# Kernel optimization log

Hardware: AMD Instinct MI355X
Metric: run time of the kernel (lower is better)

## Reference

```python
import jax, jax.numpy as jnp
import numpy as np

K = 3  # deformable kernel size
OFFSET_CLIP = 10.0


def _conv2d_same(x, w, b):
    # 3x3 conv, stride 1, padding 1, NCHW/OIHW
    out = jax.lax.conv_general_dilated(
        x, w, window_strides=(1, 1), padding=((1, 1), (1, 1)),
        dimension_numbers=("NCHW", "OIHW", "NCHW"))
    return out + b[None, :, None, None]


def _deform_conv2d(x, offset, weight):
    """torchvision-style deform_conv2d, stride 1, pad 1, dilation 1, no bias.
    x:      [B, C, H, W]
    offset: [B, 2*K*K, H, W]  (per tap: dy then dx)
    weight: [Cout, C, K, K]
    """
    B, C, H, W = x.shape
    off = offset.reshape(B, K * K, 2, H, W)
    ky, kx = jnp.meshgrid(jnp.arange(K, dtype=x.dtype), jnp.arange(K, dtype=x.dtype), indexing="ij")
    ky = ky.reshape(-1)  # [9]
    kx = kx.reshape(-1)
    # sample coords: p0 - pad + k + offset  -> [B, 9, H, W]
    ys = jnp.arange(H, dtype=x.dtype)[None, None, :, None] - 1.0 + ky[None, :, None, None] + off[:, :, 0]
    xs = jnp.arange(W, dtype=x.dtype)[None, None, None, :] - 1.0 + kx[None, :, None, None] + off[:, :, 1]
    y0 = jnp.floor(ys)
    x0 = jnp.floor(xs)
    ty = ys - y0  # fractional parts, [B,9,H,W]
    tx = xs - x0
    iy0 = y0.astype(jnp.int32)
    ix0 = x0.astype(jnp.int32)

    xf = x.reshape(B, C, H * W)

    def gather(iy, ix):
        valid = ((iy >= 0) & (iy < H) & (ix >= 0) & (ix < W)).astype(x.dtype)
        idx = (jnp.clip(iy, 0, H - 1) * W + jnp.clip(ix, 0, W - 1)).reshape(B, -1)
        v = jax.vmap(lambda xv, iv: xv[:, iv])(xf, idx)  # [B, C, 9*H*W]
        return v.reshape(B, C, K * K, H, W) * valid[:, None]

    v00 = gather(iy0, ix0)
    v01 = gather(iy0, ix0 + 1)
    v10 = gather(iy0 + 1, ix0)
    v11 = gather(iy0 + 1, ix0 + 1)

    w00 = ((1.0 - ty) * (1.0 - tx))[:, None]  # [B,1,9,H,W]
    w01 = ((1.0 - ty) * tx)[:, None]
    w10 = (ty * (1.0 - tx))[:, None]
    w11 = (ty * tx)[:, None]

    sampled = v00 * w00 + v01 * w01 + v10 * w10 + v11 * w11  # [B,C,9,H,W]
    return jnp.einsum("bckhw,ock->bohw", sampled, weight.reshape(weight.shape[0], C, K * K))


def setup_inputs() -> dict:
    key = jax.random.key(0)
    k1, k2, k3, k4 = jax.random.split(key, 4)
    B, C, H, W = 4, 64, 128, 128
    x = jax.random.normal(k1, (B, C, H, W), dtype=jnp.float32)
    ref = jax.random.normal(k2, (B, C, H, W), dtype=jnp.float32)
    # offset_conv: in=2C, out=2*3*3=18. (Original zero-inits; we use small random
    # weights so the deformable sampling path is nontrivially exercised.)
    offset_w = jax.random.normal(k3, (2 * K * K, 2 * C, K, K), dtype=jnp.float32) * 0.01
    offset_b = jnp.zeros((2 * K * K,), dtype=jnp.float32)
    # main deform weight: kaiming_normal fan_out, relu -> std = sqrt(2 / (Cout*K*K))
    std = float(np.sqrt(2.0 / (C * K * K)))
    weight = jax.random.normal(k4, (C, C, K, K), dtype=jnp.float32) * std
    return {"x": x, "ref": ref, "offset_w": offset_w, "offset_b": offset_b, "weight": weight}


def reference(x, ref, offset_w, offset_b, weight):
    combined = jnp.concatenate([x, ref], axis=1)
    offset = _conv2d_same(combined, offset_w, offset_b)
    offset = jnp.clip(offset, -OFFSET_CLIP, OFFSET_CLIP)
    aligned = _deform_conv2d(x, offset, weight)
    return aligned.astype(x.dtype)
```

## Files before the change

kernel.cpp:

```cpp
#include <hip/hip_runtime.h>

#define Bsz 4
#define Cch 64
#define Hh 128
#define Ww 128
#define NOFF 18
#define CK 576
#define CKPAD 580

typedef __attribute__((ext_vector_type(8))) short short8;
typedef __attribute__((ext_vector_type(4))) float floatx4;

__device__ __forceinline__ unsigned short f2bf(float f) {
    union { float f; unsigned u; } v; v.f = f;
    unsigned r = v.u + 0x7fff + ((v.u >> 16) & 1);
    return (unsigned short)(r >> 16);
}
__device__ __forceinline__ float bflo(unsigned d) {
    union { unsigned u; float f; } v; v.u = d << 16; return v.f;
}
__device__ __forceinline__ float bfhi(unsigned d) {
    union { unsigned u; float f; } v; v.u = d & 0xffff0000u; return v.f;
}
__device__ __forceinline__ unsigned cvtpk(float lo, float hi) {
    unsigned r;
    asm("v_cvt_pk_bf16_f32 %0, %1, %2" : "=v"(r) : "v"(lo), "v"(hi));
    return r;
}

__global__ __launch_bounds__(256) void prep(const float* __restrict__ x,
                                            const float* __restrict__ ref,
                                            const float* __restrict__ wo,
                                            const float* __restrict__ w,
                                            unsigned* __restrict__ xpair,
                                            unsigned short* __restrict__ w9,
                                            unsigned short* __restrict__ wbf) {
    __shared__ unsigned tile[64][130];
    int bid = blockIdx.x;
    int tid = threadIdx.x;
    if (bid < 512) {
        int b = bid >> 7;
        int h = bid & 127;
        int px2 = tid & 63;
        int cg = tid >> 6;
        const float* xb = x + ((size_t)b << 20) + (h << 7) + (px2 << 1);
        const float* rb = ref + ((size_t)b << 20) + (h << 7) + (px2 << 1);
#pragma unroll
        for (int j = 0; j < 16; ++j) {
            int c0 = cg * 32 + 2 * j;
            const float* s = (c0 < 64) ? xb : rb;
            int cl = c0 & 63;
            float2 va = *(const float2*)(s + ((size_t)cl << 14));
            float2 vb = *(const float2*)(s + ((size_t)(cl + 1) << 14));
            unsigned w0 = (unsigned)f2bf(va.x) | ((unsigned)f2bf(vb.x) << 16);
            unsigned w1 = (unsigned)f2bf(va.y) | ((unsigned)f2bf(vb.y) << 16);
            *(uint2*)(&tile[c0 >> 1][px2 << 1]) = make_uint2(w0, w1);
        }
        __syncthreads();
#pragma unroll
        for (int it = 0; it < 16; ++it) {
            int idx = it * 256 + tid;
            int cq5 = idx & 31;
            int pos = idx >> 5;
            int posn = min(pos + 1, 127);
            unsigned t0 = tile[2 * cq5][pos], t0n = tile[2 * cq5][posn];
            unsigned t1 = tile[2 * cq5 + 1][pos], t1n = tile[2 * cq5 + 1][posn];
            uint4 o;
            o.x = (t0 & 0xffffu) | (t0n << 16);
            o.y = (t0 >> 16) | (t0n & 0xffff0000u);
            o.z = (t1 & 0xffffu) | (t1n << 16);
            o.w = (t1 >> 16) | (t1n & 0xffff0000u);
            *(uint4*)(xpair + (((size_t)(b << 14) + (h << 7) + pos) << 7) + (cq5 << 2)) = o;
        }
    } else if (bid < 656) {
        int t = (bid - 512) * 256 + tid;
        if (t < Cch * CK) {
            int oc = t / CK;
            int rem = t % CK;
            int k = rem >> 6, c = rem & 63;
            wbf[t] = f2bf(w[(oc * Cch + c) * 9 + k]);
        }
    } else {
        int t = (bid - 656) * 256 + tid;
        if (t < 9 * 32 * 128) {
            int ci = t & 127, ocp = (t >> 7) & 31, tap = t >> 12;
            w9[t] = (ocp < NOFF) ? f2bf(wo[(ocp * 128 + ci) * 9 + tap]) : (unsigned short)0;
        }
    }
}

__global__ __launch_bounds__(256, 3) void fused_align(
        const unsigned* __restrict__ xpair,
        const unsigned short* __restrict__ w9,
        const unsigned short* __restrict__ wbf,
        const float* __restrict__ bias,
        float* __restrict__ out) {
    __shared__ union {
        unsigned short tile3[3 * 34 * 128];
        unsigned short smp[32][CKPAD];
    } u;
    __shared__ float red[2][2][64][4];
    __shared__ float4 wts[288];
    __shared__ int2 meta[288];

    int bi0 = blockIdx.x;
    int bi = ((bi0 & 7) << 8) | (bi0 >> 3);
    int b = bi >> 9;
    int rem = bi & 511;
    int h = rem >> 2;
    int w0 = (rem & 3) << 5;
    int tid = threadIdx.x;
    int wv = tid >> 6, lane = tid & 63;
    int to = wv & 1;
    int kh = wv >> 1;
    int r16 = lane & 15;
    int g = lane >> 4;

    const unsigned* xp32 = xpair + ((size_t)b << 21);

    float bias4[4] = {0.f, 0.f, 0.f, 0.f};
    if (kh == 0) {
#pragma unroll
        for (int r = 0; r < 4; ++r) {
            int oc = to * 16 + g * 4 + r;
            if (oc < NOFF) bias4[r] = bias[oc];
        }
    }

#pragma unroll
    for (int it = 0; it < 13; ++it) {
        int idx = it * 256 + tid;
        if (idx < 3264) {
            int cq4 = idx & 31;
            int pos = idx >> 5;
            int row = pos / 34, xx = pos % 34;
            int yy = h + row - 1, xg = w0 + xx - 1;
            uint4 q = make_uint4(0u, 0u, 0u, 0u);
            if ((unsigned)yy < (unsigned)Hh && (unsigned)xg < (unsigned)Ww)
                q = *(const uint4*)(xp32 + (((yy << 7) + xg) << 7) + (cq4 << 2));
            unsigned p0 = (q.x & 0xffffu) | (q.y << 16);
            unsigned p1 = (q.z & 0xffffu) | (q.w << 16);
            int ci0 = cq4 << 2;
            *(uint2*)(&u.tile3[(pos << 7) + (ci0 ^ ((xx & 7) << 3))]) = make_uint2(p0, p1);
        }
    }
    __syncthreads();

    floatx4 accA0 = {0.f, 0.f, 0.f, 0.f};
    floatx4 accA1 = {0.f, 0.f, 0.f, 0.f};
#pragma unroll
    for (int tap = 0; tap < 9; ++tap) {
        int dy = tap / 3, dx = tap % 3;
        const unsigned short* arow = w9 + ((size_t)(tap * 32 + to * 16 + r16) << 7) + kh * 64;
        short8 a0 = *(const short8*)(arow + g * 8);
        short8 a1 = *(const short8*)(arow + 32 + g * 8);
#pragma unroll
        for (int s = 0; s < 2; ++s) {
            int xxr = r16 + dx + s * 16;
            const unsigned short* brow = &u.tile3[(dy * 34 + xxr) << 7];
            int sw = (xxr & 7) << 3;
            int cb0 = kh * 64 + g * 8;
            short8 bb0 = *(const short8*)(brow + (cb0 ^ sw));
            short8 bb1 = *(const short8*)(brow + ((cb0 + 32) ^ sw));
            if (s == 0) {
                accA0 = __builtin_amdgcn_mfma_f32_16x16x32_bf16(a0, bb0, accA0, 0, 0, 0);
                accA0 = __builtin_amdgcn_mfma_f32_16x16x32_bf16(a1, bb1, accA0, 0, 0, 0);
            } else {
                accA1 = __builtin_amdgcn_mfma_f32_16x16x32_bf16(a0, bb0, accA1, 0, 0, 0);
                accA1 = __builtin_amdgcn_mfma_f32_16x16x32_bf16(a1, bb1, accA1, 0, 0, 0);
            }
        }
    }
    if (kh == 1) {
#pragma unroll
        for (int r = 0; r < 4; ++r) { red[0][to][lane][r] = accA0[r]; red[1][to][lane][r] = accA1[r]; }
    }
    __syncthreads();

    if (kh == 0 && (to == 0 || g == 0)) {
        int ntap = (to == 0) ? 2 : 1;
        int kbase = (to * 16 + g * 4) >> 1;
#pragma unroll
        for (int s = 0; s < 2; ++s) {
            float vout[4];
#pragma unroll
            for (int r = 0; r < 4; ++r) {
                float v = (s == 0 ? accA0[r] : accA1[r]) + red[s][to][lane][r] + bias4[r];
                vout[r] = fminf(fmaxf(v, -10.0f), 10.0f);
            }
            int p = s * 16 + r16;
#pragma unroll
            for (int t = 0; t < 2; ++t) {
                if (t < ntap) {
                    int k = kbase + t;
                    float dyo = vout[2 * t], dxo = vout[2 * t + 1];
                    int ky = k / 3, kx = k % 3;
                    float ys = (float)(h - 1 + ky) + dyo;
                    float xs = (float)(w0 + p - 1 + kx) + dxo;
                    float fy = floorf(ys), fx = floorf(xs);
                    int iy0 = (int)fy, ix0 = (int)fx;
                    float ty = ys - fy, tx = xs - fx;
                    float wy0 = (1.f - ty) * (((unsigned)iy0 < (unsigned)Hh) ? 1.f : 0.f);
                    float wy1 = ty         * (((unsigned)(iy0 + 1) < (unsigned)Hh) ? 1.f : 0.f);
                    float wx0 = (1.f - tx) * (((unsigned)ix0 < (unsigned)Ww) ? 1.f : 0.f);
                    float wx1 = tx         * (((unsigned)(ix0 + 1) < (unsigned)Ww) ? 1.f : 0.f);
                    int ixb  = min(max(ix0, 0), Ww - 2);
                    int iy0c = min(max(iy0, 0), Hh - 1);
                    int iy1c = min(max(iy0 + 1, 0), Hh - 1);
                    bool s0v = (min(max(ix0, 0), Ww - 1) != ixb);
                    bool s1v = (min(max(ix0 + 1, 0), Ww - 1) != ixb);
                    float w00 = wy0 * wx0, w01 = wy0 * wx1, w10 = wy1 * wx0, w11 = wy1 * wx1;
                    float A  = (s0v ? 0.f : w00) + (s1v ? 0.f : w01);
                    float Bw = (s0v ? w00 : 0.f) + (s1v ? w01 : 0.f);
                    float Cw = (s0v ? 0.f : w10) + (s1v ? 0.f : w11);
                    float Dw = (s0v ? w10 : 0.f) + (s1v ? w11 : 0.f);
                    wts[p * 9 + k] = make_float4(A, Bw, Cw, Dw);
                    meta[p * 9 + k] = make_int2(((iy0c << 7) + ixb) << 9,
                                                ((iy1c << 7) + ixb) << 9);
                }
            }
        }
    }
    __syncthreads();

    {
        int p0 = tid >> 4, cq = tid & 15;
        const char* xbB = (const char*)xpair + ((size_t)b << 23) + cq * 16;
#define GL(k, p, q0, q1, wt, mm)                                                      \
        float4 wt = wts[(p) * 9 + (k)]; int2 mm = meta[(p) * 9 + (k)];                \
        uint4 q0 = *(const uint4*)(xbB + mm.x);                                       \
        uint4 q1 = *(const uint4*)(xbB + mm.y);
#define CP(k, p, q0, q1, wt) {                                                        \
        float s0 = bflo(q0.x)*wt.x + bfhi(q0.x)*wt.y + bflo(q1.x)*wt.z + bfhi(q1.x)*wt.w; \
        float s1 = bflo(q0.y)*wt.x + bfhi(q0.y)*wt.y + bflo(q1.y)*wt.z + bfhi(q1.y)*wt.w; \
        float s2 = bflo(q0.z)*wt.x + bfhi(q0.z)*wt.y + bflo(q1.z)*wt.z + bfhi(q1.z)*wt.w; \
        float s3 = bflo(q0.w)*wt.x + bfhi(q0.w)*wt.y + bflo(q1.w)*wt.z + bfhi(q1.w)*wt.w; \
        *(uint2*)(&u.smp[p][(k) * 64 + cq * 4]) = make_uint2(cvtpk(s0, s1), cvtpk(s2, s3)); }
#pragma unroll
        for (int s = 0; s < 2; ++s) {
            int p = p0 + s * 16;
            GL(0, p, a0, a1, wA, mA)
            GL(1, p, b0, b1, wB, mB)
            GL(2, p, c0, c1, wC, mC)
            CP(0, p, a0, a1, wA)
            CP(1, p, b0, b1, wB)
            CP(2, p, c0, c1, wC)
            GL(3, p, d0, d1, wD, mD)
            GL(4, p, e0, e1, wE, mE)
            GL(5, p, f0, f1, wF, mF)
            CP(3, p, d0, d1, wD)
            CP(4, p, e0, e1, wE)
            CP(5, p, f0, f1, wF)
            GL(6, p, g0, g1, wG, mG)
            GL(7, p, h0, h1, wH, mH)
            GL(8, p, i0, i1, wI, mI)
            CP(6, p, g0, g1, wG)
            CP(7, p, h0, h1, wH)
            CP(8, p, i0, i1, wI)
        }
#undef GL
#undef CP
    }
    __syncthreads();

    {
        floatx4 acc0 = {0.f, 0.f, 0.f, 0.f};
        floatx4 acc1 = {0.f, 0.f, 0.f, 0.f};
        const short8* ap = (const short8*)(wbf + (size_t)(wv * 16 + r16) * CK + g * 8);
        const unsigned short* bb0 = &u.smp[r16][g * 8];
        const unsigned short* bb1 = &u.smp[16 + r16][g * 8];
#pragma unroll
        for (int kk = 0; kk < 18; ++kk) {
            short8 a = ap[kk * 4];
            short8 v0 = *(const short8*)(bb0 + kk * 32);
            short8 v1 = *(const short8*)(bb1 + kk * 32);
            acc0 = __builtin_amdgcn_mfma_f32_16x16x32_bf16(a, v0, acc0, 0, 0, 0);
            acc1 = __builtin_amdgcn_mfma_f32_16x16x32_bf16(a, v1, acc1, 0, 0, 0);
        }
        size_t obase = ((size_t)(b * Cch + wv * 16 + g * 4)) << 14;
        int hw = (h << 7) + w0 + r16;
#pragma unroll
        for (int r = 0; r < 4; ++r) {
            out[obase + ((size_t)r << 14) + hw] = acc0[r];
            out[obase + ((size_t)r << 14) + hw + 16] = acc1[r];
        }
    }
}

extern "C" void kernel_launch(void* const* d_in, const int* in_sizes, int n_in,
                              void* d_out, int out_size, void* d_ws, size_t ws_size,
                              hipStream_t stream) {
    const float* x      = (const float*)d_in[0];
    const float* ref    = (const float*)d_in[1];
    const float* wo     = (const float*)d_in[2];
    const float* bias   = (const float*)d_in[3];
    const float* weight = (const float*)d_in[4];
    float* out = (float*)d_out;

    unsigned short* w9  = (unsigned short*)d_ws;
    unsigned short* wbf = (unsigned short*)((char*)d_ws + 262144);
    unsigned* xpair     = (unsigned*)((char*)d_ws + 524288);

    hipLaunchKernelGGL(prep, dim3(800), dim3(256), 0, stream,
                       x, ref, wo, weight, xpair, w9, wbf);
    hipLaunchKernelGGL(fused_align, dim3(2048), dim3(256), 0, stream,
                       xpair, w9, wbf, bias, out);
}
```

Baseline: 78.01 us.

## Halve sampled-tile LDS footprint and preload weight fragments to raise occupancy

The bilinear-sampled tile buffer now holds 16 pixels instead of 32 and is processed in two passes, each followed by its own MFMA and output store. The wts/meta arrays move into the shared-memory union, and the A-operand weight fragments are loaded once into registers (18 short8) before the loop. Launch bounds go from 3 to 4 blocks per CU. The aim is a smaller LDS footprint so more blocks fit per CU. The cost is extra __syncthreads between passes, less overlap between sampling and MFMA, and higher register pressure from the preloaded weights under the tighter launch bound.

```diff
diff --git a/kernel.cpp b/kernel.cpp
--- a/kernel.cpp
+++ b/kernel.cpp
@@ -89,7 +89,7 @@
     }
 }
 
-__global__ __launch_bounds__(256, 3) void fused_align(
+__global__ __launch_bounds__(256, 4) void fused_align(
         const unsigned* __restrict__ xpair,
         const unsigned short* __restrict__ w9,
         const unsigned short* __restrict__ wbf,
@@ -97,11 +97,13 @@
         float* __restrict__ out) {
     __shared__ union {
         unsigned short tile3[3 * 34 * 128];
-        unsigned short smp[32][CKPAD];
+        struct {
+            unsigned short smp[16][CKPAD];
+            float4 wts[288];
+            int2 meta[288];
+        } bb;
     } u;
     __shared__ float red[2][2][64][4];
-    __shared__ float4 wts[288];
-    __shared__ int2 meta[288];
 
     int bi0 = blockIdx.x;
     int bi = ((bi0 & 7) << 8) | (bi0 >> 3);
@@ -214,76 +216,77 @@
                     float Bw = (s0v ? w00 : 0.f) + (s1v ? w01 : 0.f);
                     float Cw = (s0v ? 0.f : w10) + (s1v ? 0.f : w11);
                     float Dw = (s0v ? w10 : 0.f) + (s1v ? w11 : 0.f);
-                    wts[p * 9 + k] = make_float4(A, Bw, Cw, Dw);
-                    meta[p * 9 + k] = make_int2(((iy0c << 7) + ixb) << 9,
-                                                ((iy1c << 7) + ixb) << 9);
+                    u.bb.wts[p * 9 + k] = make_float4(A, Bw, Cw, Dw);
+                    u.bb.meta[p * 9 + k] = make_int2(((iy0c << 7) + ixb) << 9,
+                                                     ((iy1c << 7) + ixb) << 9);
                 }
             }
         }
     }
     __syncthreads();
 
+    short8 areg[18];
     {
-        int p0 = tid >> 4, cq = tid & 15;
-        const char* xbB = (const char*)xpair + ((size_t)b << 23) + cq * 16;
-#define GL(k, p, q0, q1, wt, mm)                                                      \
-        float4 wt = wts[(p) * 9 + (k)]; int2 mm = meta[(p) * 9 + (k)];                \
-        uint4 q0 = *(const uint4*)(xbB + mm.x);                                       \
-        uint4 q1 = *(const uint4*)(xbB + mm.y);
-#define CP(k, p, q0, q1, wt) {                                                        \
-        float s0 = bflo(q0.x)*wt.x + bfhi(q0.x)*wt.y + bflo(q1.x)*wt.z + bfhi(q1.x)*wt.w; \
-        float s1 = bflo(q0.y)*wt.x + bfhi(q0.y)*wt.y + bflo(q1.y)*wt.z + bfhi(q1.y)*wt.w; \
-        float s2 = bflo(q0.z)*wt.x + bfhi(q0.z)*wt.y + bflo(q1.z)*wt.z + bfhi(q1.z)*wt.w; \
-        float s3 = bflo(q0.w)*wt.x + bfhi(q0.w)*wt.y + bflo(q1.w)*wt.z + bfhi(q1.w)*wt.w; \
-        *(uint2*)(&u.smp[p][(k) * 64 + cq * 4]) = make_uint2(cvtpk(s0, s1), cvtpk(s2, s3)); }
-#pragma unroll
-        for (int s = 0; s < 2; ++s) {
+        const short8* ap = (const short8*)(wbf + (size_t)(wv * 16 + r16) * CK + g * 8);
+#pragma unroll
+        for (int kk = 0; kk < 18; ++kk) areg[kk] = ap[kk * 4];
+    }
+
+    int p0 = tid >> 4, cq = tid & 15;
+    const char* xbB = (const char*)xpair + ((size_t)b << 23) + cq * 16;
+    int hwbase = (h << 7) + w0 + r16;
+    size_t obase = ((size_t)(b * Cch + wv * 16 + g * 4)) << 14;
+
+#pragma unroll
+    for (int s = 0; s < 2; ++s) {
+        {
             int p = p0 + s * 16;
-            GL(0, p, a0, a1, wA, mA)
-            GL(1, p, b0, b1, wB, mB)
-            GL(2, p, c0, c1, wC, mC)
-            CP(0, p, a0, a1, wA)
-            CP(1, p, b0, b1, wB)
-            CP(2, p, c0, c1, wC)
-            GL(3, p, d0, d1, wD, mD)
-            GL(4, p, e0, e1, wE, mE)
-            GL(5, p, f0, f1, wF, mF)
-            CP(3, p, d0, d1, wD)
-            CP(4, p, e0, e1, wE)
-            CP(5, p, f0, f1, wF)
-            GL(6, p, g0, g1, wG, mG)
-            GL(7, p, h0, h1, wH, mH)
-            GL(8, p, i0, i1, wI, mI)
-            CP(6, p, g0, g1, wG)
-            CP(7, p, h0, h1, wH)
-            CP(8, p, i0, i1, wI)
-        }
+#define GL(k, q0, q1, wt, mm)                                                         \
+            float4 wt = u.bb.wts[p * 9 + (k)]; int2 mm = u.bb.meta[p * 9 + (k)];      \
+            uint4 q0 = *(const uint4*)(xbB + mm.x);                                   \
+            uint4 q1 = *(const uint4*)(xbB + mm.y);
+#define CP(k, q0, q1, wt) {                                                           \
+            float s0 = bflo(q0.x)*wt.x + bfhi(q0.x)*wt.y + bflo(q1.x)*wt.z + bfhi(q1.x)*wt.w; \
+            float s1 = bflo(q0.y)*wt.x + bfhi(q0.y)*wt.y + bflo(q1.y)*wt.z + bfhi(q1.y)*wt.w; \
+            float s2 = bflo(q0.z)*wt.x + bfhi(q0.z)*wt.y + bflo(q1.z)*wt.z + bfhi(q1.z)*wt.w; \
+            float s3 = bflo(q0.w)*wt.x + bfhi(q0.w)*wt.y + bflo(q1.w)*wt.z + bfhi(q1.w)*wt.w; \
+            *(uint2*)(&u.bb.smp[p0][(k) * 64 + cq * 4]) =                             \
+                make_uint2(cvtpk(s0, s1), cvtpk(s2, s3)); }
+            GL(0, a0, a1, wA, mA)
+            GL(1, b0, b1, wB, mB)
+            GL(2, c0, c1, wC, mC)
+            CP(0, a0, a1, wA)
+            CP(1, b0, b1, wB)
+            CP(2, c0, c1, wC)
+            GL(3, d0, d1, wD, mD)
+            GL(4, e0, e1, wE, mE)
+            GL(5, f0, f1, wF, mF)
+            CP(3, d0, d1, wD)
+            CP(4, e0, e1, wE)
+            CP(5, f0, f1, wF)
+            GL(6, g0, g1, wG, mG)
+            GL(7, h0, h1, wH, mH)
+            GL(8, i0, i1, wI, mI)
+            CP(6, g0, g1, wG)
+            CP(7, h0, h1, wH)
+            CP(8, i0, i1, wI)
 #undef GL
 #undef CP
-    }
-    __syncthreads();
-
-    {
-        floatx4 acc0 = {0.f, 0.f, 0.f, 0.f};
-        floatx4 acc1 = {0.f, 0.f, 0.f, 0.f};
-        const short8* ap = (const short8*)(wbf + (size_t)(wv * 16 + r16) * CK + g * 8);
-        const unsigned short* bb0 = &u.smp[r16][g * 8];
-        const unsigned short* bb1 = &u.smp[16 + r16][g * 8];
+        }
+        __syncthreads();
+
+        floatx4 acc = {0.f, 0.f, 0.f, 0.f};
+        const unsigned short* bbase = &u.bb.smp[r16][g * 8];
 #pragma unroll
         for (int kk = 0; kk < 18; ++kk) {
-            short8 a = ap[kk * 4];
-            short8 v0 = *(const short8*)(bb0 + kk * 32);
-            short8 v1 = *(const short8*)(bb1 + kk * 32);
-            acc0 = __builtin_amdgcn_mfma_f32_16x16x32_bf16(a, v0, acc0, 0, 0, 0);
-            acc1 = __builtin_amdgcn_mfma_f32_16x16x32_bf16(a, v1, acc1, 0, 0, 0);
-        }
-        size_t obase = ((size_t)(b * Cch + wv * 16 + g * 4)) << 14;
-        int hw = (h << 7) + w0 + r16;
-#pragma unroll
-        for (int r = 0; r < 4; ++r) {
-            out[obase + ((size_t)r << 14) + hw] = acc0[r];
-            out[obase + ((size_t)r << 14) + hw + 16] = acc1[r];
-        }
+            short8 v = *(const short8*)(bbase + kk * 32);
+            acc = __builtin_amdgcn_mfma_f32_16x16x32_bf16(areg[kk], v, acc, 0, 0, 0);
+        }
+        int hw = hwbase + s * 16;
+#pragma unroll
+        for (int r = 0; r < 4; ++r)
+            out[obase + ((size_t)r << 14) + hw] = acc[r];
+        if (s == 0) __syncthreads();
     }
 }
 
```

Measured after the change: 83.81 us. +7.4%, slower.
